# Performance work log

Measured on AMD Instinct MI355X. Metric: run time of the kernel, lower is better.

Reference implementation:

```python
import jax, jax.numpy as jnp
import numpy as np

N = 262144   # number of samples
C = 16       # GMM components
D = 64       # feature dim


def setup_inputs() -> dict:
    key = jax.random.key(0)
    k1, k2, k3, k4 = jax.random.split(key, 4)
    inputs = jax.random.normal(k1, (N, D), dtype=jnp.float32)
    # SPD inverse covariances, as produced by inverting fitted GMM covariances
    R = jax.random.normal(k2, (C, D, D), dtype=jnp.float32)
    covariances_inv = jnp.einsum('cij,ckj->cik', R, R) / D + 0.1 * jnp.eye(D, dtype=jnp.float32)
    means = jax.random.normal(k3, (C, D), dtype=jnp.float32)
    w = jax.random.uniform(k4, (C,), dtype=jnp.float32, minval=0.1, maxval=1.0)
    weights = w / jnp.sum(w)  # mixture weights sum to 1
    return {"inputs": inputs, "covariances_inv": covariances_inv,
            "means": means, "weights": weights}


def reference(inputs, covariances_inv, means, weights):
    # Mahalanobis quadratic form per component: d[n,c] = (x_n - m_c)^T Sigma_c^{-1} (x_n - m_c)
    centered = inputs[:, None, :] - means[None, :, :]                # [N, C, D]
    distances_sqr = jnp.einsum('ncd,cde,nce->nc', centered, covariances_inv, centered)  # [N, C]
    # score_n = prod_c d[n,c] ** w_c
    score = jnp.prod(distances_sqr ** weights[None, :], axis=1)      # [N]
    return score
```

## Files before the change

kernel.cpp:

```cpp
#include <hip/hip_runtime.h>

typedef __attribute__((ext_vector_type(4))) float f32x4;
typedef __attribute__((ext_vector_type(8))) short bf16x8;

__device__ __forceinline__ short f2bf(float f) {
    union { float f; unsigned u; } v; v.f = f;
    unsigned u = v.u + 0x7FFFu + ((v.u >> 16) & 1u);
    return (short)(u >> 16);
}
__device__ __forceinline__ int pack_bf2(float a, float b) {
    union { float f; unsigned u; } ua, ub; ua.f = a; ub.f = b;
    unsigned x = ua.u + 0x8000u, y = ub.u + 0x8000u;
    return (int)__builtin_amdgcn_perm(y, x, 0x07060302u);
}
__device__ __forceinline__ float bflo(int p) {
    union { int i; float f; } v; v.i = p << 16; return v.f;
}
__device__ __forceinline__ float bfhi(int p) {
    union { int i; float f; } v; v.i = p & 0xffff0000; return v.f;
}

__global__ void gmm_prep(const float* __restrict__ Ainv,
                         const float* __restrict__ means,
                         short* __restrict__ AbP16,
                         float* __restrict__ biasP,
                         float* __restrict__ kscal) {
    __shared__ float sA[64 * 68];
    __shared__ float sm[64];
    __shared__ float sb[64];
    const int c = blockIdx.x, t = threadIdx.x;
    const float* A = Ainv + c * 4096;
    #pragma unroll
    for (int i = 0; i < 4; ++i) {
        int flat = i * 1024 + t * 4;
        int r = flat >> 6, col = flat & 63;
        *(f32x4*)&sA[r * 68 + col] = *(const f32x4*)(A + flat);
    }
    if (t < 64) sm[t] = means[c * 64 + t];
    __syncthreads();
    {
        int j = t >> 2, seg = t & 3;
        float p = 0.f;
        #pragma unroll
        for (int k = 0; k < 16; ++k) p += sA[j * 68 + seg * 16 + k] * sm[seg * 16 + k];
        p += __shfl_xor(p, 1, 64); p += __shfl_xor(p, 2, 64);
        if ((t & 3) == 0) sb[j] = p;
    }
    __syncthreads();
    if (t < 64) {
        float km = sm[t] * sb[t];
        #pragma unroll
        for (int off = 32; off >= 1; off >>= 1) km += __shfl_xor(km, off, 64);
        if (t == 0) kscal[c] = km;
        int rt = t >> 4, qh = (t >> 2) & 3, r = t & 3;
        int pj = (rt >> 1) * 32 + 8 * qh + 4 * (rt & 1) + r;
        biasP[c * 64 + t] = -2.f * sb[pj];
    }
    #pragma unroll
    for (int rep = 0; rep < 2; ++rep) {
        int f = rep * 256 + t;
        int rt = f >> 7, kc = (f >> 6) & 1, L = f & 63;
        int ln = L & 15, q = L >> 4;
        int pj = (rt >> 1) * 32 + 8 * (ln >> 2) + 4 * (rt & 1) + (ln & 3);
        const float* src = &sA[pj * 68 + 32 * kc + 8 * q];
        bf16x8 v;
        #pragma unroll
        for (int j = 0; j < 8; ++j) v[j] = f2bf(src[j]);
        *(bf16x8*)(AbP16 + c * 4096 + f * 8) = v;
    }
}

union BFrag { bf16x8 v; int i[4]; };

__global__ __launch_bounds__(256) void gmm_main(
    const float* __restrict__ X,
    const float* __restrict__ weights,
    const short* __restrict__ AbP16,
    const float* __restrict__ biasP,
    const float* __restrict__ kscal,
    float* __restrict__ out) {

    __shared__ short sAb[16384];
    __shared__ float sBias[16 * 64];
    __shared__ float sKW[32];

    const int tid = threadIdx.x;
    const int lane = tid & 63, w = tid >> 6;
    const int q = lane >> 4, ln = lane & 15;
    const int base = blockIdx.x * 256 + w * 64;

    #pragma unroll
    for (int i = 0; i < 8; ++i)
        ((int4*)sAb)[i * 256 + tid] = ((const int4*)AbP16)[i * 256 + tid];
    ((f32x4*)sBias)[tid] = ((const f32x4*)biasP)[tid];
    if (tid < 16) { sKW[tid] = kscal[tid]; sKW[16 + tid] = weights[tid]; }

    BFrag xb[4][2];
    #pragma unroll
    for (int t = 0; t < 4; ++t) {
        const float* xr = X + (size_t)(base + t * 16 + ln) * 64 + 8 * q;
        #pragma unroll
        for (int kc = 0; kc < 2; ++kc) {
            f32x4 a = *(const f32x4*)(xr + 32 * kc);
            f32x4 b = *(const f32x4*)(xr + 32 * kc + 4);
            xb[t][kc].i[0] = pack_bf2(a[0], a[1]);
            xb[t][kc].i[1] = pack_bf2(a[2], a[3]);
            xb[t][kc].i[2] = pack_bf2(b[0], b[1]);
            xb[t][kc].i[3] = pack_bf2(b[2], b[3]);
        }
    }
    __syncthreads();

    float slog[4] = {0.f, 0.f, 0.f, 0.f};

    #pragma unroll 1
    for (int g = 0; g < 4; ++g) {
        #pragma unroll 1
        for (int cl = 0; cl < 4; ++cl) {
            const int c = g * 4 + cl;
            bf16x8 af[8];
            #pragma unroll
            for (int f = 0; f < 8; ++f)
                af[f] = *(const bf16x8*)&sAb[cl * 4096 + f * 512 + lane * 8];
            f32x4 bias[4];
            #pragma unroll
            for (int rt = 0; rt < 4; ++rt)
                bias[rt] = *(const f32x4*)&sBias[c * 64 + rt * 16 + q * 4];
            const float kc_ = sKW[c], wcc = sKW[16 + c];

            #pragma unroll
            for (int t = 0; t < 4; ++t) {
                float dp = 0.f;
                #pragma unroll
                for (int rt = 0; rt < 4; ++rt) {
                    f32x4 acc = __builtin_amdgcn_mfma_f32_16x16x32_bf16(
                        af[rt * 2 + 0], xb[t][0].v, bias[rt], 0, 0, 0);
                    acc = __builtin_amdgcn_mfma_f32_16x16x32_bf16(
                        af[rt * 2 + 1], xb[t][1].v, acc, 0, 0, 0);
                    int pa = xb[t][rt >> 1].i[(rt & 1) * 2];
                    int pb = xb[t][rt >> 1].i[(rt & 1) * 2 + 1];
                    dp += acc[0] * bflo(pa) + acc[1] * bfhi(pa)
                        + acc[2] * bflo(pb) + acc[3] * bfhi(pb);
                }
                dp += __shfl_xor(dp, 16, 64);
                dp += __shfl_xor(dp, 32, 64);
                float d = fmaxf(dp + kc_, 1e-30f);
                slog[t] = fmaf(wcc, __builtin_amdgcn_logf(d), slog[t]);
            }
        }
        if (g < 3) {
            __syncthreads();
            const int4* src = (const int4*)(AbP16 + (g + 1) * 16384);
            #pragma unroll
            for (int i = 0; i < 8; ++i)
                ((int4*)sAb)[i * 256 + tid] = src[i * 256 + tid];
            __syncthreads();
        }
    }

    if (q == 0) {
        #pragma unroll
        for (int t = 0; t < 4; ++t)
            out[base + t * 16 + ln] = __builtin_amdgcn_exp2f(slog[t]);
    }
}

extern "C" void kernel_launch(void* const* d_in, const int* in_sizes, int n_in,
                              void* d_out, int out_size, void* d_ws, size_t ws_size,
                              hipStream_t stream) {
    const float* X       = (const float*)d_in[0];
    const float* Ainv    = (const float*)d_in[1];
    const float* means   = (const float*)d_in[2];
    const float* weights = (const float*)d_in[3];
    float* out = (float*)d_out;
    const int N = in_sizes[0] / 64;

    short* AbP16 = (short*)d_ws;
    float* biasP = (float*)((char*)d_ws + 131072);
    float* kscal = (float*)((char*)d_ws + 135168);

    gmm_prep<<<dim3(16), dim3(256), 0, stream>>>(Ainv, means, AbP16, biasP, kscal);
    gmm_main<<<dim3(N / 256), dim3(256), 0, stream>>>(X, weights, AbP16, biasP, kscal, out);
}
```

Before: 132.4 us.

## Use Cholesky factor so quadratic form becomes sum of squares via 32x32 MFMA

The prep kernel now Cholesky-factors each inverse covariance, so x^T A x becomes ||L^T x||^2. Main then squares MFMA outputs directly instead of dotting the results back against x. The linear term -2 A m · x is precomputed once per block for all components with a separate MFMA into shared memory. It also switches to 32x32x16 MFMA tiles and staggers the component-group order per block. The serial 64-step Cholesky loop in prep adds latency and can change bf16 rounding error, but the main loop does less ALU work per component.

```diff
diff --git a/kernel.cpp b/kernel.cpp
--- a/kernel.cpp
+++ b/kernel.cpp
@@ -1,7 +1,8 @@
 #include <hip/hip_runtime.h>
 
-typedef __attribute__((ext_vector_type(4))) float f32x4;
-typedef __attribute__((ext_vector_type(8))) short bf16x8;
+typedef __attribute__((ext_vector_type(4)))  float f32x4;
+typedef __attribute__((ext_vector_type(16))) float f32x16;
+typedef __attribute__((ext_vector_type(8)))  short bf16x8;
 
 __device__ __forceinline__ short f2bf(float f) {
     union { float f; unsigned u; } v; v.f = f;
@@ -13,17 +14,11 @@
     unsigned x = ua.u + 0x8000u, y = ub.u + 0x8000u;
     return (int)__builtin_amdgcn_perm(y, x, 0x07060302u);
 }
-__device__ __forceinline__ float bflo(int p) {
-    union { int i; float f; } v; v.i = p << 16; return v.f;
-}
-__device__ __forceinline__ float bfhi(int p) {
-    union { int i; float f; } v; v.i = p & 0xffff0000; return v.f;
-}
 
 __global__ void gmm_prep(const float* __restrict__ Ainv,
                          const float* __restrict__ means,
-                         short* __restrict__ AbP16,
-                         float* __restrict__ biasP,
+                         short* __restrict__ LtF,
+                         short* __restrict__ Bb32,
                          float* __restrict__ kscal) {
     __shared__ float sA[64 * 68];
     __shared__ float sm[64];
@@ -52,21 +47,53 @@
         #pragma unroll
         for (int off = 32; off >= 1; off >>= 1) km += __shfl_xor(km, off, 64);
         if (t == 0) kscal[c] = km;
-        int rt = t >> 4, qh = (t >> 2) & 3, r = t & 3;
-        int pj = (rt >> 1) * 32 + 8 * qh + 4 * (rt & 1) + r;
-        biasP[c * 64 + t] = -2.f * sb[pj];
+        #pragma unroll
+        for (int kc = 0; kc < 4; ++kc) {
+            if ((t & 31) == c) {
+                bf16x8 v;
+                #pragma unroll
+                for (int j = 0; j < 8; ++j)
+                    v[j] = f2bf(-2.f * sb[kc * 16 + (t >> 5) * 8 + j]);
+                *(bf16x8*)(Bb32 + kc * 512 + t * 8) = v;
+            }
+            if (c == 0 && (t & 31) >= 16) {
+                bf16x8 z;
+                #pragma unroll
+                for (int j = 0; j < 8; ++j) z[j] = 0;
+                *(bf16x8*)(Bb32 + kc * 512 + t * 8) = z;
+            }
+        }
+    }
+    const int r = t >> 2, s = t & 3;
+    for (int k = 0; k < 64; ++k) {
+        float dk = sA[k * 68 + k];
+        float sq = sqrtf(dk), inv = 1.0f / sq;
+        __syncthreads();
+        if (s == 0 && r >= k)
+            sA[r * 68 + k] = (r == k) ? sq : sA[r * 68 + k] * inv;
+        __syncthreads();
+        if (r > k) {
+            float lrk = sA[r * 68 + k];
+            int j0 = (k + 1 > s * 16) ? k + 1 : s * 16;
+            int j1 = (r < s * 16 + 15) ? r : s * 16 + 15;
+            for (int j = j0; j <= j1; ++j)
+                sA[r * 68 + j] -= lrk * sA[j * 68 + k];
+        }
+        __syncthreads();
     }
     #pragma unroll
     for (int rep = 0; rep < 2; ++rep) {
-        int f = rep * 256 + t;
-        int rt = f >> 7, kc = (f >> 6) & 1, L = f & 63;
-        int ln = L & 15, q = L >> 4;
-        int pj = (rt >> 1) * 32 + 8 * (ln >> 2) + 4 * (rt & 1) + (ln & 3);
-        const float* src = &sA[pj * 68 + 32 * kc + 8 * q];
+        int idx = rep * 256 + t;
+        int f = idx >> 6, L = idx & 63;
+        int m = (f >> 2) * 32 + (L & 31);
+        int kb = (f & 3) * 16 + (L >> 5) * 8;
         bf16x8 v;
         #pragma unroll
-        for (int j = 0; j < 8; ++j) v[j] = f2bf(src[j]);
-        *(bf16x8*)(AbP16 + c * 4096 + f * 8) = v;
+        for (int j = 0; j < 8; ++j) {
+            int k = kb + j;
+            v[j] = (m <= k) ? f2bf(sA[k * 68 + m]) : (short)0;
+        }
+        *(bf16x8*)(LtF + c * 4096 + f * 512 + L * 8) = v;
     }
 }
 
@@ -75,82 +102,107 @@
 __global__ __launch_bounds__(256) void gmm_main(
     const float* __restrict__ X,
     const float* __restrict__ weights,
-    const short* __restrict__ AbP16,
-    const float* __restrict__ biasP,
+    const short* __restrict__ LtF,
+    const short* __restrict__ Bb32,
     const float* __restrict__ kscal,
     float* __restrict__ out) {
 
     __shared__ short sAb[16384];
-    __shared__ float sBias[16 * 64];
+    __shared__ float sLin[16 * 256];
     __shared__ float sKW[32];
 
     const int tid = threadIdx.x;
     const int lane = tid & 63, w = tid >> 6;
-    const int q = lane >> 4, ln = lane & 15;
+    const int h = lane >> 5, col = lane & 31;
     const int base = blockIdx.x * 256 + w * 64;
-
+    const int boff = blockIdx.x & 3;
+
+    {
+        const int4* src = (const int4*)LtF + boff * 2048;
+        #pragma unroll
+        for (int i = 0; i < 8; ++i)
+            ((int4*)sAb)[i * 256 + tid] = src[i * 256 + tid];
+    }
+    if (tid < 16) { sKW[tid] = kscal[tid]; sKW[16 + tid] = weights[tid]; }
+
+    BFrag xb[2][4];
     #pragma unroll
-    for (int i = 0; i < 8; ++i)
-        ((int4*)sAb)[i * 256 + tid] = ((const int4*)AbP16)[i * 256 + tid];
-    ((f32x4*)sBias)[tid] = ((const f32x4*)biasP)[tid];
-    if (tid < 16) { sKW[tid] = kscal[tid]; sKW[16 + tid] = weights[tid]; }
-
-    BFrag xb[4][2];
-    #pragma unroll
-    for (int t = 0; t < 4; ++t) {
-        const float* xr = X + (size_t)(base + t * 16 + ln) * 64 + 8 * q;
-        #pragma unroll
-        for (int kc = 0; kc < 2; ++kc) {
-            f32x4 a = *(const f32x4*)(xr + 32 * kc);
-            f32x4 b = *(const f32x4*)(xr + 32 * kc + 4);
+    for (int t = 0; t < 2; ++t) {
+        const float* xr = X + (size_t)(base + t * 32 + col) * 64 + h * 8;
+        #pragma unroll
+        for (int kc = 0; kc < 4; ++kc) {
+            f32x4 a = *(const f32x4*)(xr + kc * 16);
+            f32x4 b = *(const f32x4*)(xr + kc * 16 + 4);
             xb[t][kc].i[0] = pack_bf2(a[0], a[1]);
             xb[t][kc].i[1] = pack_bf2(a[2], a[3]);
             xb[t][kc].i[2] = pack_bf2(b[0], b[1]);
             xb[t][kc].i[3] = pack_bf2(b[2], b[3]);
         }
     }
+
+    {
+        bf16x8 bb[4];
+        #pragma unroll
+        for (int kc = 0; kc < 4; ++kc)
+            bb[kc] = *(const bf16x8*)(Bb32 + kc * 512 + lane * 8);
+        #pragma unroll
+        for (int t = 0; t < 2; ++t) {
+            f32x16 acc;
+            #pragma unroll
+            for (int i = 0; i < 16; ++i) acc[i] = 0.f;
+            #pragma unroll
+            for (int kc = 0; kc < 4; ++kc)
+                acc = __builtin_amdgcn_mfma_f32_32x32x16_bf16(
+                    bb[kc], xb[t][kc].v, acc, 0, 0, 0);
+            #pragma unroll
+            for (int rg = 0; rg < 8; ++rg) {
+                int row = (rg & 3) + 8 * (rg >> 2) + 4 * h;
+                sLin[row * 256 + w * 64 + t * 32 + col] = acc[rg];
+            }
+        }
+    }
     __syncthreads();
 
-    float slog[4] = {0.f, 0.f, 0.f, 0.f};
+    float slog[2] = {0.f, 0.f};
 
     #pragma unroll 1
-    for (int g = 0; g < 4; ++g) {
+    for (int gi = 0; gi < 4; ++gi) {
+        const int g = (gi + boff) & 3;
         #pragma unroll 1
         for (int cl = 0; cl < 4; ++cl) {
-            const int c = g * 4 + cl;
             bf16x8 af[8];
             #pragma unroll
             for (int f = 0; f < 8; ++f)
                 af[f] = *(const bf16x8*)&sAb[cl * 4096 + f * 512 + lane * 8];
-            f32x4 bias[4];
-            #pragma unroll
-            for (int rt = 0; rt < 4; ++rt)
-                bias[rt] = *(const f32x4*)&sBias[c * 64 + rt * 16 + q * 4];
+            const int c = g * 4 + cl;
             const float kc_ = sKW[c], wcc = sKW[16 + c];
-
-            #pragma unroll
-            for (int t = 0; t < 4; ++t) {
+            const float* lp = sLin + c * 256 + w * 64 + col;
+
+            #pragma unroll
+            for (int t = 0; t < 2; ++t) {
+                f32x16 a0, a1;
+                #pragma unroll
+                for (int i = 0; i < 16; ++i) { a0[i] = 0.f; a1[i] = 0.f; }
+                #pragma unroll
+                for (int kc = 0; kc < 4; ++kc)
+                    a0 = __builtin_amdgcn_mfma_f32_32x32x16_bf16(
+                        af[kc], xb[t][kc].v, a0, 0, 0, 0);
+                #pragma unroll
+                for (int kc = 0; kc < 4; ++kc)
+                    a1 = __builtin_amdgcn_mfma_f32_32x32x16_bf16(
+                        af[4 + kc], xb[t][kc].v, a1, 0, 0, 0);
                 float dp = 0.f;
                 #pragma unroll
-                for (int rt = 0; rt < 4; ++rt) {
-                    f32x4 acc = __builtin_amdgcn_mfma_f32_16x16x32_bf16(
-                        af[rt * 2 + 0], xb[t][0].v, bias[rt], 0, 0, 0);
-                    acc = __builtin_amdgcn_mfma_f32_16x16x32_bf16(
-                        af[rt * 2 + 1], xb[t][1].v, acc, 0, 0, 0);
-                    int pa = xb[t][rt >> 1].i[(rt & 1) * 2];
-                    int pb = xb[t][rt >> 1].i[(rt & 1) * 2 + 1];
-                    dp += acc[0] * bflo(pa) + acc[1] * bfhi(pa)
-                        + acc[2] * bflo(pb) + acc[3] * bfhi(pb);
-                }
-                dp += __shfl_xor(dp, 16, 64);
+                for (int i = 0; i < 16; ++i)
+                    dp += a0[i] * a0[i] + a1[i] * a1[i];
                 dp += __shfl_xor(dp, 32, 64);
-                float d = fmaxf(dp + kc_, 1e-30f);
+                float d = fmaxf(dp + lp[t * 32] + kc_, 1e-30f);
                 slog[t] = fmaf(wcc, __builtin_amdgcn_logf(d), slog[t]);
             }
         }
-        if (g < 3) {
+        if (gi < 3) {
             __syncthreads();
-            const int4* src = (const int4*)(AbP16 + (g + 1) * 16384);
+            const int4* src = (const int4*)LtF + (((gi + 1 + boff) & 3) * 2048);
             #pragma unroll
             for (int i = 0; i < 8; ++i)
                 ((int4*)sAb)[i * 256 + tid] = src[i * 256 + tid];
@@ -158,10 +210,10 @@
         }
     }
 
-    if (q == 0) {
-        #pragma unroll
-        for (int t = 0; t < 4; ++t)
-            out[base + t * 16 + ln] = __builtin_amdgcn_exp2f(slog[t]);
+    if (lane < 32) {
+        #pragma unroll
+        for (int t = 0; t < 2; ++t)
+            out[base + t * 32 + lane] = __builtin_amdgcn_exp2f(slog[t]);
     }
 }
 
@@ -175,10 +227,10 @@
     float* out = (float*)d_out;
     const int N = in_sizes[0] / 64;
 
-    short* AbP16 = (short*)d_ws;
-    float* biasP = (float*)((char*)d_ws + 131072);
+    short* LtF   = (short*)d_ws;
+    short* Bb32  = (short*)((char*)d_ws + 131072);
     float* kscal = (float*)((char*)d_ws + 135168);
 
-    gmm_prep<<<dim3(16), dim3(256), 0, stream>>>(Ainv, means, AbP16, biasP, kscal);
-    gmm_main<<<dim3(N / 256), dim3(256), 0, stream>>>(X, weights, AbP16, biasP, kscal, out);
-}
+    gmm_prep<<<dim3(16), dim3(256), 0, stream>>>(Ainv, means, LtF, Bb32, kscal);
+    gmm_main<<<dim3(N / 256), dim3(256), 0, stream>>>(X, weights, LtF, Bb32, kscal, out);
+}
```

Result: slower. 190.8 us (+44.1%).
